# Kernel tuning notes

Measured on AMD Instinct MI355X. Metric: run time of the kernel, lower is better.

Reference implementation:

```python
import jax, jax.numpy as jnp
import numpy as np

B, M, D, OUT = 16384, 4096, 512, 128


def setup_inputs() -> dict:
    key = jax.random.key(0)
    ks = jax.random.split(key, 5)
    x = jax.random.normal(ks[0], (B, D), dtype=jnp.float32)
    support = jax.random.normal(ks[1], (M, D), dtype=jnp.float32)
    gamma = jnp.float32(1.0)
    head_w = jax.random.normal(ks[2], (OUT, M), dtype=jnp.float32) / np.sqrt(M)
    head_b = jax.random.normal(ks[3], (OUT,), dtype=jnp.float32) * 0.01
    scale = jnp.ones((1,), dtype=jnp.float32)
    shift = jnp.zeros((1,), dtype=jnp.float32)
    return {"x": x, "support": support, "gamma": gamma,
            "head_w": head_w, "head_b": head_b,
            "scale": scale, "shift": shift}


def reference(x, support, gamma, head_w, head_b, scale, shift):
    x2 = jnp.sum(x * x, axis=-1, keepdims=True)           # [B, 1]
    s2 = jnp.sum(support * support, axis=-1)              # [M]
    xs = jnp.einsum('bd,md->bm', x, support)              # [B, M]
    sqdist = jnp.maximum(x2 + s2[None, :] - 2.0 * xs, 0.0)
    k = jnp.exp(-gamma * sqdist)                          # RBF kernel [B, M]
    out = jnp.einsum('bm,om->bo', k, head_w) + head_b     # linear head [B, OUT]
    return scale * out + shift
```

## Files before the change

### kernel.cpp

```cpp
#include <hip/hip_runtime.h>

typedef unsigned int u32;
typedef unsigned short u16;
typedef unsigned char u8;
typedef __attribute__((ext_vector_type(8))) __bf16 bf16x8;
typedef __attribute__((ext_vector_type(4))) float f32x4;
typedef __attribute__((ext_vector_type(4))) int i32x4;

#define NB 16384
#define NM 4096
#define ND 512
#define NOUT 128
#define L2E 1.44269504088896340736f


#define WAITLG(N) do { asm volatile("s_waitcnt vmcnt(" #N ") lgkmcnt(0)" ::: "memory"); \
                       __builtin_amdgcn_sched_barrier(0); } while (0)
#define LGKM0() do { asm volatile("s_waitcnt lgkmcnt(0)" ::: "memory"); \
                     __builtin_amdgcn_sched_barrier(0); } while (0)
#define SB0() __builtin_amdgcn_sched_barrier(0)

__device__ __forceinline__ u16 f2bf(float f) {
  u32 u = __float_as_uint(f);
  u += 0x7FFFu + ((u >> 16) & 1u);
  return (u16)(u >> 16);
}

__device__ __forceinline__ u8 f2fp8(float f) {
  u32 u = __float_as_uint(f);
  u32 s = (u >> 24) & 0x80u;
  u32 au = u & 0x7FFFFFFFu;
  if (au < 0x3C800000u) return (u8)s;
  au += 0x000FFFFFu + ((au >> 20) & 1u);
  u32 e = (au >> 23) - 120u;
  u32 m = (au >> 20) & 7u;
  return (u8)(s | (e << 3) | m);
}

__device__ __forceinline__ void stage16(const void* g, void* l) {
  __builtin_amdgcn_global_load_lds((__attribute__((address_space(1))) void*)g,
                                   (__attribute__((address_space(3))) void*)l,
                                   16, 0, 0);
}

__device__ __forceinline__ bf16x8 ldg_b128(const void* p) {
  i32x4 r;
  asm volatile("global_load_dwordx4 %0, %1, off" : "=&v"(r) : "v"(p) : "memory");
  return __builtin_bit_cast(bf16x8, r);
}

__device__ __forceinline__ uint4 pack8bf(float4 v0, float4 v1) {
  uint4 pk;
  pk.x = (u32)f2bf(v0.x) | ((u32)f2bf(v0.y) << 16);
  pk.y = (u32)f2bf(v0.z) | ((u32)f2bf(v0.w) << 16);
  pk.z = (u32)f2bf(v1.x) | ((u32)f2bf(v1.y) << 16);
  pk.w = (u32)f2bf(v1.z) | ((u32)f2bf(v1.w) << 16);
  return pk;
}

__device__ __forceinline__ uint2 pack8f8(float4 v0, float4 v1) {
  uint2 pk;
  pk.x = (u32)f2fp8(v0.x) | ((u32)f2fp8(v0.y) << 8) |
         ((u32)f2fp8(v0.z) << 16) | ((u32)f2fp8(v0.w) << 24);
  pk.y = (u32)f2fp8(v1.x) | ((u32)f2fp8(v1.y) << 8) |
         ((u32)f2fp8(v1.z) << 16) | ((u32)f2fp8(v1.w) << 24);
  return pk;
}

__global__ __launch_bounds__(256) void prep_all(const float* __restrict__ x,
                                                const float* __restrict__ s,
                                                const float* __restrict__ hw,
                                                const float* __restrict__ gamma_p,
                                                u8*  __restrict__ x_ws,
                                                u8*  __restrict__ s_ws,
                                                u16* __restrict__ hw_ws,
                                                float* __restrict__ x2g,
                                                float* __restrict__ s2g,
                                                float* __restrict__ out) {
  __shared__ uint2 t8[2048];
  __shared__ uint4 t16[2048];
  const int tid = threadIdx.x, bid = blockIdx.x;
  const int lane = tid & 63, w = tid >> 6;

  if (bid < 640) {
    const bool isx = bid < 512;
    const int blk = isx ? bid : (bid - 512);
    const float* src_m = isx ? x : s;
    u8*    dst_ws = isx ? x_ws : s_ws;
    float* sq_out = isx ? x2g : s2g;
    const float gl   = gamma_p[0] * L2E;
    const float cmul = isx ? 1.0f : (-2.0f * gl);
    const int big  = isx ? (blk >> 1) : (blk >> 2);
    const int roff = isx ? ((blk & 1) * 32) : ((blk & 3) * 32);
    const int rows = isx ? 64 : 128;

    #pragma unroll
    for (int p = 0; p < 8; ++p) {
      const int row = p * 4 + w;
      const float* src = src_m + (size_t)(blk * 32 + row) * ND + lane * 8;
      float4 v0 = *(const float4*)src;
      float4 v1 = *(const float4*)(src + 4);
      float ss = v0.x*v0.x + v0.y*v0.y + v0.z*v0.z + v0.w*v0.w
               + v1.x*v1.x + v1.y*v1.y + v1.z*v1.z + v1.w*v1.w;
      #pragma unroll
      for (int off = 32; off > 0; off >>= 1) ss += __shfl_down(ss, off);
      if (lane == 0) sq_out[blk * 32 + row] = gl * ss;
      v0.x *= cmul; v0.y *= cmul; v0.z *= cmul; v0.w *= cmul;
      v1.x *= cmul; v1.y *= cmul; v1.z *= cmul; v1.w *= cmul;
      t8[lane * 32 + ((row + lane) & 31)] = pack8f8(v0, v1);
    }
    __syncthreads();
    #pragma unroll
    for (int p = 0; p < 8; ++p) {
      const int kg = p * 8 + (tid >> 5);
      const int row = tid & 31;
      uint2 pk = t8[kg * 32 + ((row + kg) & 31)];
      *(uint2*)&dst_ws[(((size_t)(big * 64 + kg)) * rows + roff + row) * 8] = pk;
    }
  } else if (bid < 672) {
    const int blk = bid - 640;
    #pragma unroll
    for (int p = 0; p < 8; ++p) {
      const int o = p * 16 + (tid >> 4);
      const int kg = tid & 15;
      const float* src = hw + (size_t)o * NM + blk * 128 + kg * 8;
      float4 v0 = *(const float4*)src;
      float4 v1 = *(const float4*)(src + 4);
      t16[o * 16 + ((kg + o) & 15)] = pack8bf(v0, v1);
    }
    __syncthreads();
    #pragma unroll
    for (int it = 0; it < 8; ++it) {
      const int kg = it * 2 + (tid >> 7);
      const int o = tid & 127;
      uint4 pk = t16[o * 16 + ((kg + o) & 15)];
      *(uint4*)&hw_ws[(((size_t)(blk * 16 + kg)) * 128 + o) * 8] = pk;
    }
  } else {
    float4* o4 = (float4*)out;
    const float4 z = {0.f, 0.f, 0.f, 0.f};
    size_t base = (size_t)(bid - 672) * 8192 + tid;
    #pragma unroll 8
    for (int i = 0; i < 32; ++i) o4[base + (size_t)i * 256] = z;
  }
}

__global__ __launch_bounds__(256, 2)
void rbf_fused(const u8* __restrict__ x_ws, const u8* __restrict__ s_ws,
               const u16* __restrict__ hw_ws, const float* __restrict__ x2g,
               const float* __restrict__ s2g, const float* __restrict__ head_b,
               const float* __restrict__ scale_p, const float* __restrict__ shift_p,
               float* __restrict__ out)
{
  extern __shared__ __align__(16) char smem[];

  const int tid  = threadIdx.x;
  const int w    = tid >> 6;
  const int lane = tid & 63;
  const int quad = lane >> 4;
  const int l16  = lane & 15;
  const int wr   = w & 1;
  const int wc   = w >> 1;
  const int xcd  = blockIdx.x & 7;
  const int rb   = (blockIdx.x >> 3) * 2 + (xcd & 1);
  const int half = xcd >> 1;
  const int b0   = rb * 64;

  const float vscale = scale_p[0];
  const float vshift = shift_p[0];

  const u8* xsrc = x_ws + (size_t)rb * 32768;
  const u8* ssrc = s_ws + (size_t)(half * 8) * 65536;

  auto stage_tile = [&](int j) {
    const u8* sp = ssrc + (size_t)(j >> 3) * 65536 + (j & 7) * 8192;
    char* dp = smem + (j & 7) * 8192;
    stage16(sp + tid * 16, dp + tid * 16);
    stage16(sp + 4096 + tid * 16, dp + 4096 + tid * 16);
  };

  auto rdB = [&](int buf, int kcL, long long* dst) {
    #pragma unroll
    for (int c = 0; c < 4; ++c)
      dst[c] = *(const long long*)(smem + buf * 8192 +
                ((kcL * 4 + quad) * 128 + wc * 64 + c * 16 + l16) * 8);
  };

  f32x4 x2v[2];
  #pragma unroll
  for (int r = 0; r < 2; ++r)
    x2v[r] = *(const f32x4*)&x2g[b0 + wr * 32 + r * 16 + quad * 4];
  SB0();
  long long aX[16][2];
  #pragma unroll
  for (int kc = 0; kc < 16; ++kc)
    #pragma unroll
    for (int r = 0; r < 2; ++r)
      aX[kc][r] = *(const long long*)(xsrc + ((kc * 4 + quad) * 64 + wr * 32 + r * 16 + l16) * 8);
  SB0();
  #pragma unroll
  for (int j = 0; j < 6; ++j) stage_tile(j);
  asm volatile("s_waitcnt vmcnt(6)" ::: "memory");
  SB0();
  __builtin_amdgcn_s_barrier();
  SB0();

  long long bF0[4], bF1[4];
  rdB(0, 0, bF0);
  LGKM0();

  const f32x4 zf = {0.f, 0.f, 0.f, 0.f};
  f32x4 acc_xs[2][4];
  f32x4 acc_out[2][4];
  #pragma unroll
  for (int r = 0; r < 2; ++r)
    #pragma unroll
    for (int c = 0; c < 4; ++c) { acc_xs[r][c] = zf; acc_out[r][c] = zf; }

  bf16x8 b2[2][4];

  #pragma unroll 1
  for (int mt = 0; mt < 8; ++mt) {
    const int mtg = half * 8 + mt;
    float s2v[4];

    #pragma unroll
    for (int s = 0; s < 4; ++s) {
      if (s == 0) {
        #pragma unroll
        for (int c = 0; c < 4; ++c)
          s2v[c] = s2g[mtg * 128 + wc * 64 + c * 16 + l16];
        SB0();
      }
      bf16x8 a2[2];

      __builtin_amdgcn_s_setprio(1);
      #pragma unroll
      for (int r = 0; r < 2; ++r)
        #pragma unroll
        for (int c = 0; c < 4; ++c)
          acc_xs[r][c] = __builtin_amdgcn_mfma_f32_16x16x32_fp8_fp8(
              aX[s * 4 + 0][r], bF0[c], acc_xs[r][c], 0, 0, 0);
      __builtin_amdgcn_s_setprio(0);
      SB0();
      rdB(2 * s, 1, bF1);
      if (mt > 0) {
        const int kg = s * 4 + quad;
        #pragma unroll
        for (int r = 0; r < 2; ++r)
          a2[r] = *(const bf16x8*)(smem + 65536 + (kg * 64 + wr * 32 + r * 16 + l16) * 16);
      }
      LGKM0();

      __builtin_amdgcn_s_setprio(1);
      #pragma unroll
      for (int r = 0; r < 2; ++r)
        #pragma unroll
        for (int c = 0; c < 4; ++c)
          acc_xs[r][c] = __builtin_amdgcn_mfma_f32_16x16x32_fp8_fp8(
              aX[s * 4 + 1][r], bF1[c], acc_xs[r][c], 0, 0, 0);
      __builtin_amdgcn_s_setprio(0);
      SB0();
      rdB(2 * s + 1, 0, bF0);
      LGKM0();

      __builtin_amdgcn_s_setprio(1);
      #pragma unroll
      for (int r = 0; r < 2; ++r)
        #pragma unroll
        for (int c = 0; c < 4; ++c)
          acc_xs[r][c] = __builtin_amdgcn_mfma_f32_16x16x32_fp8_fp8(
              aX[s * 4 + 2][r], bF0[c], acc_xs[r][c], 0, 0, 0);
      __builtin_amdgcn_s_setprio(0);
      SB0();
      rdB(2 * s + 1, 1, bF1);
      LGKM0();

      __builtin_amdgcn_s_setprio(1);
      #pragma unroll
      for (int r = 0; r < 2; ++r)
        #pragma unroll
        for (int c = 0; c < 4; ++c)
          acc_xs[r][c] = __builtin_amdgcn_mfma_f32_16x16x32_fp8_fp8(
              aX[s * 4 + 3][r], bF1[c], acc_xs[r][c], 0, 0, 0);
      __builtin_amdgcn_s_setprio(0);
      SB0();
      if (!(mt == 7 && s == 3)) rdB((2 * s + 2) & 7, 0, bF0);
      LGKM0();

      if (mt > 0) {
        __builtin_amdgcn_s_setprio(1);
        #pragma unroll
        for (int r = 0; r < 2; ++r)
          #pragma unroll
          for (int c = 0; c < 4; ++c)
            acc_out[r][c] = __builtin_amdgcn_mfma_f32_16x16x32_bf16(
                a2[r], b2[s & 1][c], acc_out[r][c], 0, 0, 0);
        __builtin_amdgcn_s_setprio(0);
      }
      SB0();

      if (s == 0 || mt < 7) {
        const int j = mt * 8 + 2 * s + 6;
        stage_tile(j);
        stage_tile(j + 1);
      }
      SB0();

      if ((s <= 1) ? (mt >= 1) : (mt <= 6)) {
        const int umt = mt + (s >= 2);
        const int us  = (s + 2) & 3;
        const size_t sb = (size_t)((half * 8 + umt - 1) * 16 + us * 4 + quad);
        #pragma unroll
        for (int c = 0; c < 4; ++c)
          b2[s & 1][c] = ldg_b128(hw_ws + (sb * 128 + wc * 64 + c * 16 + l16) * 8);
      }

      if (mt == 0)      { if (s == 0) WAITLG(10); else if (s == 1) WAITLG(4); else WAITLG(8); }
      else if (mt < 7)  { if (s == 0) WAITLG(12); else WAITLG(8); }
      else              { if (s == 0) WAITLG(12); else if (s == 1) WAITLG(4); else WAITLG(0); }
      __builtin_amdgcn_s_barrier();
      SB0();
    }

    {
      #pragma unroll
      for (int r = 0; r < 2; ++r)
        #pragma unroll
        for (int c = 0; c < 4; ++c) {
          const int cl = wc * 64 + c * 16 + l16;
          char* kbase = smem + 65536 + (cl >> 3) * 1024 + (cl & 7) * 2;
          #pragma unroll
          for (int i = 0; i < 4; ++i) {
            const int row = wr * 32 + r * 16 + quad * 4 + i;
            const float t = acc_xs[r][c][i] + x2v[r][i] + s2v[c];
            float kv = __builtin_amdgcn_exp2f(-t);
            kv = fminf(kv, 1.0f);
            *(u16*)(kbase + row * 16) = (u16)(__float_as_uint(kv) >> 16);
            acc_xs[r][c][i] = 0.0f;
          }
        }
    }
    LGKM0();
    __builtin_amdgcn_s_barrier();
    SB0();
  }

  #pragma unroll
  for (int ks = 0; ks < 4; ++ks) {
    const int kg = ks * 4 + quad;
    const size_t sb = (size_t)((half * 8 + 7) * 16 + kg);
    bf16x8 bb[4], a2[2];
    #pragma unroll
    for (int c = 0; c < 4; ++c)
      bb[c] = *(const bf16x8*)(hw_ws + (sb * 128 + wc * 64 + c * 16 + l16) * 8);
    #pragma unroll
    for (int r = 0; r < 2; ++r)
      a2[r] = *(const bf16x8*)(smem + 65536 + (kg * 64 + wr * 32 + r * 16 + l16) * 16);
    #pragma unroll
    for (int r = 0; r < 2; ++r)
      #pragma unroll
      for (int c = 0; c < 4; ++c)
        acc_out[r][c] = __builtin_amdgcn_mfma_f32_16x16x32_bf16(a2[r], bb[c], acc_out[r][c], 0, 0, 0);
  }

  float addv[4];
  #pragma unroll
  for (int c = 0; c < 4; ++c) {
    const int col = wc * 64 + c * 16 + l16;
    addv[c] = (half == 0) ? (vscale * head_b[col] + vshift) : 0.0f;
  }
  #pragma unroll
  for (int r = 0; r < 2; ++r)
    #pragma unroll
    for (int c = 0; c < 4; ++c) {
      const int col = wc * 64 + c * 16 + l16;
      #pragma unroll
      for (int i = 0; i < 4; ++i) {
        const int row = b0 + wr * 32 + r * 16 + quad * 4 + i;
        atomicAdd(&out[(size_t)row * NOUT + col], vscale * acc_out[r][c][i] + addv[c]);
      }
    }
}

extern "C" void kernel_launch(void* const* d_in, const int* in_sizes, int n_in,
                              void* d_out, int out_size, void* d_ws, size_t ws_size,
                              hipStream_t stream) {
  const float* x       = (const float*)d_in[0];
  const float* support = (const float*)d_in[1];
  const float* gamma   = (const float*)d_in[2];
  const float* head_w  = (const float*)d_in[3];
  const float* head_b  = (const float*)d_in[4];
  const float* scale   = (const float*)d_in[5];
  const float* shift   = (const float*)d_in[6];
  float* out = (float*)d_out;

  char* w = (char*)d_ws;
  u8*    x_ws  = (u8*)(w);
  u8*    s_ws  = (u8*)(w + 8388608);
  u16*   hw_ws = (u16*)(w + 10485760);
  float* x2g   = (float*)(w + 11534336);
  float* s2g   = (float*)(w + 11599872);

  static bool lds_init = false;
  if (!lds_init) {
    hipFuncSetAttribute(reinterpret_cast<const void*>(rbf_fused),
                        hipFuncAttributeMaxDynamicSharedMemorySize, 81920);
    lds_init = true;
  }

  prep_all<<<736, 256, 0, stream>>>(x, support, head_w, gamma,
                                    x_ws, s_ws, hw_ws, x2g, s2g, out);
  rbf_fused<<<1024, 256, 81920, stream>>>(x_ws, s_ws, hw_ws, x2g, s2g,
                                          head_b, scale, shift, out);
}
```

Before: 187.9 us.

## Stage x tile in LDS and double-buffer A/B fragments across sub-steps

The x tile is now staged into LDS instead of being held in 32 registers per lane. Support tiles use a 4-slot ring instead of 8. The A and B fragments are double-buffered in registers: fragments for the next sub-step are read from LDS while the current MFMAs run, which removes the per-MFMA-group lgkmcnt(0) stalls. Global staging and head-weight loads move to the top of each sub-step, and the tuned vmcnt waits become a full vmcnt(0) wait before each barrier. This frees registers and overlaps LDS reads, but adds LDS traffic for x and may expose global-load latency at every barrier.

Result: slower. 221.7 us (+18.0%).

```diff
diff --git a/kernel.cpp b/kernel.cpp
--- a/kernel.cpp
+++ b/kernel.cpp
@@ -16,7 +16,7 @@
 
 #define WAITLG(N) do { asm volatile("s_waitcnt vmcnt(" #N ") lgkmcnt(0)" ::: "memory"); \
                        __builtin_amdgcn_sched_barrier(0); } while (0)
-#define LGKM0() do { asm volatile("s_waitcnt lgkmcnt(0)" ::: "memory"); \
+#define LGKM(N) do { asm volatile("s_waitcnt lgkmcnt(" #N ")" ::: "memory"); \
                      __builtin_amdgcn_sched_barrier(0); } while (0)
 #define SB0() __builtin_amdgcn_sched_barrier(0)
 
@@ -174,40 +174,46 @@
 
   auto stage_tile = [&](int j) {
     const u8* sp = ssrc + (size_t)(j >> 3) * 65536 + (j & 7) * 8192;
-    char* dp = smem + (j & 7) * 8192;
+    char* dp = smem + 32768 + (j & 3) * 8192;
     stage16(sp + tid * 16, dp + tid * 16);
     stage16(sp + 4096 + tid * 16, dp + 4096 + tid * 16);
   };
 
-  auto rdB = [&](int buf, int kcL, long long* dst) {
-    #pragma unroll
-    for (int c = 0; c < 4; ++c)
-      dst[c] = *(const long long*)(smem + buf * 8192 +
-                ((kcL * 4 + quad) * 128 + wc * 64 + c * 16 + l16) * 8);
-  };
-
   f32x4 x2v[2];
   #pragma unroll
   for (int r = 0; r < 2; ++r)
     x2v[r] = *(const f32x4*)&x2g[b0 + wr * 32 + r * 16 + quad * 4];
   SB0();
-  long long aX[16][2];
-  #pragma unroll
-  for (int kc = 0; kc < 16; ++kc)
-    #pragma unroll
-    for (int r = 0; r < 2; ++r)
-      aX[kc][r] = *(const long long*)(xsrc + ((kc * 4 + quad) * 64 + wr * 32 + r * 16 + l16) * 8);
+  #pragma unroll
+  for (int i = 0; i < 8; ++i)
+    stage16(xsrc + i * 4096 + tid * 16, smem + i * 4096 + tid * 16);
   SB0();
   #pragma unroll
-  for (int j = 0; j < 6; ++j) stage_tile(j);
-  asm volatile("s_waitcnt vmcnt(6)" ::: "memory");
+  for (int j = 0; j < 4; ++j) stage_tile(j);
+  asm volatile("s_waitcnt vmcnt(4)" ::: "memory");
   SB0();
   __builtin_amdgcn_s_barrier();
   SB0();
 
-  long long bF0[4], bF1[4];
-  rdB(0, 0, bF0);
-  LGKM0();
+  long long aF[2][4][2];
+  long long bF[2][4][4];
+  bf16x8 b2[2][4];
+  bf16x8 a2[2];
+
+  #pragma unroll
+  for (int i = 0; i < 4; ++i)
+    #pragma unroll
+    for (int r = 0; r < 2; ++r)
+      aF[0][i][r] = *(const long long*)(smem + ((i * 4 + quad) * 64 + wr * 32 + r * 16 + l16) * 8);
+  #pragma unroll
+  for (int i = 0; i < 4; ++i)
+    #pragma unroll
+    for (int c = 0; c < 4; ++c)
+      bF[0][i][c] = *(const long long*)(smem + 32768 + (i >> 1) * 8192 +
+                     (((i & 1) * 4 + quad) * 128 + wc * 64 + c * 16 + l16) * 8);
+  LGKM(0);
+  __builtin_amdgcn_s_barrier();
+  SB0();
 
   const f32x4 zf = {0.f, 0.f, 0.f, 0.f};
   f32x4 acc_xs[2][4];
@@ -216,8 +222,6 @@
   for (int r = 0; r < 2; ++r)
     #pragma unroll
     for (int c = 0; c < 4; ++c) { acc_xs[r][c] = zf; acc_out[r][c] = zf; }
-
-  bf16x8 b2[2][4];
 
   #pragma unroll 1
   for (int mt = 0; mt < 8; ++mt) {
@@ -226,13 +230,34 @@
 
     #pragma unroll
     for (int s = 0; s < 4; ++s) {
+      const int p  = s & 1;
+      const int pn = p ^ 1;
+      const int sN = (s + 1) & 3;
+      const bool doRd = !(mt == 7 && s == 3);
+      const bool doSt = (mt * 4 + s) <= 29;
+
       if (s == 0) {
         #pragma unroll
         for (int c = 0; c < 4; ++c)
           s2v[c] = s2g[mtg * 128 + wc * 64 + c * 16 + l16];
         SB0();
       }
-      bf16x8 a2[2];
+      if (doSt) {
+        const int j = (mt * 4 + s) * 2 + 4;
+        stage_tile(j);
+        stage_tile(j + 1);
+      }
+      SB0();
+      if ((s < 3 && mt >= 1) || (s == 3 && mt <= 6)) {
+        const int um = (s < 3) ? mt : (mt + 1);
+        const size_t sb = (size_t)((half * 8 + um - 1) * 16 + sN * 4 + quad);
+        #pragma unroll
+        for (int c = 0; c < 4; ++c)
+          b2[sN & 1][c] = ldg_b128(hw_ws + (sb * 128 + wc * 64 + c * 16 + l16) * 8);
+      }
+      SB0();
+
+      const int jn = (mt * 4 + s) * 2 + 2;
 
       __builtin_amdgcn_s_setprio(1);
       #pragma unroll
@@ -240,85 +265,99 @@
         #pragma unroll
         for (int c = 0; c < 4; ++c)
           acc_xs[r][c] = __builtin_amdgcn_mfma_f32_16x16x32_fp8_fp8(
-              aX[s * 4 + 0][r], bF0[c], acc_xs[r][c], 0, 0, 0);
+              aF[p][0][r], bF[p][0][c], acc_xs[r][c], 0, 0, 0);
       __builtin_amdgcn_s_setprio(0);
       SB0();
-      rdB(2 * s, 1, bF1);
+      if (doRd) {
+        #pragma unroll
+        for (int i = 0; i < 2; ++i)
+          #pragma unroll
+          for (int r = 0; r < 2; ++r)
+            aF[pn][i][r] = *(const long long*)(smem +
+                (((sN * 4 + i) * 4 + quad) * 64 + wr * 32 + r * 16 + l16) * 8);
+        #pragma unroll
+        for (int c = 0; c < 4; ++c)
+          bF[pn][0][c] = *(const long long*)(smem + 32768 + (jn & 3) * 8192 +
+              ((0 * 4 + quad) * 128 + wc * 64 + c * 16 + l16) * 8);
+      }
+      SB0();
+
+      __builtin_amdgcn_s_setprio(1);
+      #pragma unroll
+      for (int r = 0; r < 2; ++r)
+        #pragma unroll
+        for (int c = 0; c < 4; ++c)
+          acc_xs[r][c] = __builtin_amdgcn_mfma_f32_16x16x32_fp8_fp8(
+              aF[p][1][r], bF[p][1][c], acc_xs[r][c], 0, 0, 0);
+      __builtin_amdgcn_s_setprio(0);
+      SB0();
+      if (doRd) {
+        #pragma unroll
+        for (int c = 0; c < 4; ++c)
+          bF[pn][1][c] = *(const long long*)(smem + 32768 + (jn & 3) * 8192 +
+              ((1 * 4 + quad) * 128 + wc * 64 + c * 16 + l16) * 8);
+        #pragma unroll
+        for (int i = 2; i < 4; ++i)
+          #pragma unroll
+          for (int r = 0; r < 2; ++r)
+            aF[pn][i][r] = *(const long long*)(smem +
+                (((sN * 4 + i) * 4 + quad) * 64 + wr * 32 + r * 16 + l16) * 8);
+      }
+      SB0();
+
+      __builtin_amdgcn_s_setprio(1);
+      #pragma unroll
+      for (int r = 0; r < 2; ++r)
+        #pragma unroll
+        for (int c = 0; c < 4; ++c)
+          acc_xs[r][c] = __builtin_amdgcn_mfma_f32_16x16x32_fp8_fp8(
+              aF[p][2][r], bF[p][2][c], acc_xs[r][c], 0, 0, 0);
+      __builtin_amdgcn_s_setprio(0);
+      SB0();
+      if (doRd) {
+        #pragma unroll
+        for (int c = 0; c < 4; ++c)
+          bF[pn][2][c] = *(const long long*)(smem + 32768 + ((jn + 1) & 3) * 8192 +
+              ((0 * 4 + quad) * 128 + wc * 64 + c * 16 + l16) * 8);
+      }
+      SB0();
+
+      __builtin_amdgcn_s_setprio(1);
+      #pragma unroll
+      for (int r = 0; r < 2; ++r)
+        #pragma unroll
+        for (int c = 0; c < 4; ++c)
+          acc_xs[r][c] = __builtin_amdgcn_mfma_f32_16x16x32_fp8_fp8(
+              aF[p][3][r], bF[p][3][c], acc_xs[r][c], 0, 0, 0);
+      __builtin_amdgcn_s_setprio(0);
+      SB0();
       if (mt > 0) {
         const int kg = s * 4 + quad;
         #pragma unroll
         for (int r = 0; r < 2; ++r)
           a2[r] = *(const bf16x8*)(smem + 65536 + (kg * 64 + wr * 32 + r * 16 + l16) * 16);
       }
-      LGKM0();
-
-      __builtin_amdgcn_s_setprio(1);
-      #pragma unroll
-      for (int r = 0; r < 2; ++r)
-        #pragma unroll
-        for (int c = 0; c < 4; ++c)
-          acc_xs[r][c] = __builtin_amdgcn_mfma_f32_16x16x32_fp8_fp8(
-              aX[s * 4 + 1][r], bF1[c], acc_xs[r][c], 0, 0, 0);
-      __builtin_amdgcn_s_setprio(0);
-      SB0();
-      rdB(2 * s + 1, 0, bF0);
-      LGKM0();
-
-      __builtin_amdgcn_s_setprio(1);
-      #pragma unroll
-      for (int r = 0; r < 2; ++r)
-        #pragma unroll
-        for (int c = 0; c < 4; ++c)
-          acc_xs[r][c] = __builtin_amdgcn_mfma_f32_16x16x32_fp8_fp8(
-              aX[s * 4 + 2][r], bF0[c], acc_xs[r][c], 0, 0, 0);
-      __builtin_amdgcn_s_setprio(0);
-      SB0();
-      rdB(2 * s + 1, 1, bF1);
-      LGKM0();
-
-      __builtin_amdgcn_s_setprio(1);
-      #pragma unroll
-      for (int r = 0; r < 2; ++r)
-        #pragma unroll
-        for (int c = 0; c < 4; ++c)
-          acc_xs[r][c] = __builtin_amdgcn_mfma_f32_16x16x32_fp8_fp8(
-              aX[s * 4 + 3][r], bF1[c], acc_xs[r][c], 0, 0, 0);
-      __builtin_amdgcn_s_setprio(0);
-      SB0();
-      if (!(mt == 7 && s == 3)) rdB((2 * s + 2) & 7, 0, bF0);
-      LGKM0();
+      if (doRd) {
+        #pragma unroll
+        for (int c = 0; c < 4; ++c)
+          bF[pn][3][c] = *(const long long*)(smem + 32768 + ((jn + 1) & 3) * 8192 +
+              ((1 * 4 + quad) * 128 + wc * 64 + c * 16 + l16) * 8);
+      }
+      SB0();
 
       if (mt > 0) {
+        if (doRd) { LGKM(4); } else { LGKM(0); }
         __builtin_amdgcn_s_setprio(1);
         #pragma unroll
         for (int r = 0; r < 2; ++r)
           #pragma unroll
           for (int c = 0; c < 4; ++c)
             acc_out[r][c] = __builtin_amdgcn_mfma_f32_16x16x32_bf16(
-                a2[r], b2[s & 1][c], acc_out[r][c], 0, 0, 0);
+                a2[r], b2[p][c], acc_out[r][c], 0, 0, 0);
         __builtin_amdgcn_s_setprio(0);
       }
-      SB0();
-
-      if (s == 0 || mt < 7) {
-        const int j = mt * 8 + 2 * s + 6;
-        stage_tile(j);
-        stage_tile(j + 1);
-      }
-      SB0();
-
-      if ((s <= 1) ? (mt >= 1) : (mt <= 6)) {
-        const int umt = mt + (s >= 2);
-        const int us  = (s + 2) & 3;
-        const size_t sb = (size_t)((half * 8 + umt - 1) * 16 + us * 4 + quad);
-        #pragma unroll
-        for (int c = 0; c < 4; ++c)
-          b2[s & 1][c] = ldg_b128(hw_ws + (sb * 128 + wc * 64 + c * 16 + l16) * 8);
-      }
-
-      if (mt == 0)      { if (s == 0) WAITLG(10); else if (s == 1) WAITLG(4); else WAITLG(8); }
-      else if (mt < 7)  { if (s == 0) WAITLG(12); else WAITLG(8); }
-      else              { if (s == 0) WAITLG(12); else if (s == 1) WAITLG(4); else WAITLG(0); }
+
+      WAITLG(0);
       __builtin_amdgcn_s_barrier();
       SB0();
     }
@@ -341,7 +380,7 @@
           }
         }
     }
-    LGKM0();
+    LGKM(0);
     __builtin_amdgcn_s_barrier();
     SB0();
   }
@@ -350,18 +389,18 @@
   for (int ks = 0; ks < 4; ++ks) {
     const int kg = ks * 4 + quad;
     const size_t sb = (size_t)((half * 8 + 7) * 16 + kg);
-    bf16x8 bb[4], a2[2];
+    bf16x8 bb[4], aa[2];
     #pragma unroll
     for (int c = 0; c < 4; ++c)
       bb[c] = *(const bf16x8*)(hw_ws + (sb * 128 + wc * 64 + c * 16 + l16) * 8);
     #pragma unroll
     for (int r = 0; r < 2; ++r)
-      a2[r] = *(const bf16x8*)(smem + 65536 + (kg * 64 + wr * 32 + r * 16 + l16) * 16);
+      aa[r] = *(const bf16x8*)(smem + 65536 + (kg * 64 + wr * 32 + r * 16 + l16) * 16);
     #pragma unroll
     for (int r = 0; r < 2; ++r)
       #pragma unroll
       for (int c = 0; c < 4; ++c)
-        acc_out[r][c] = __builtin_amdgcn_mfma_f32_16x16x32_bf16(a2[r], bb[c], acc_out[r][c], 0, 0, 0);
+        acc_out[r][c] = __builtin_amdgcn_mfma_f32_16x16x32_bf16(aa[r], bb[c], acc_out[r][c], 0, 0, 0);
   }
 
   float addv[4];
```
